# Optimization experiments

Measured on AMD Instinct MI355X. Metric: run time of the kernel, lower is better.

The kernel has to match this reference:

```python
import jax, jax.numpy as jnp
import numpy as np

N_NODES = 50000
N_EDGES = 800000
NODE_DIM = 64
EDGE_DIM = 32
OUT_FEATS = 64


def setup_inputs() -> dict:
    key = jax.random.key(0)
    k1, k2, k3, k4, k5, k6, k7 = jax.random.split(key, 7)
    node_features = jax.random.normal(k1, (N_NODES, NODE_DIM), dtype=jnp.float32)
    edge_features = jax.random.normal(k2, (N_EDGES, EDGE_DIM), dtype=jnp.float32)
    src = jax.random.randint(k3, (N_EDGES,), 0, N_NODES, dtype=jnp.int32)
    dst = jax.random.randint(k4, (N_EDGES,), 0, N_NODES, dtype=jnp.int32)
    in_dim = 2 * NODE_DIM + EDGE_DIM  # concat([e_ft, h_src, h_dst])
    w_group = jax.random.normal(k5, (in_dim,), dtype=jnp.float32) * 0.05
    w_srcattn = jax.random.normal(k6, (NODE_DIM + EDGE_DIM,), dtype=jnp.float32) * 0.05
    w_lin = jax.random.normal(k7, (in_dim, OUT_FEATS), dtype=jnp.float32) * 0.05
    return {"node_features": node_features, "edge_features": edge_features,
            "src": src, "dst": dst,
            "w_group": w_group, "w_srcattn": w_srcattn, "w_lin": w_lin}


def _segment_softmax(scores, seg, num_segments):
    # numerically-stable softmax of per-edge scalar scores within each segment
    m = jax.ops.segment_max(scores, seg, num_segments=num_segments)
    e = jnp.exp(scores - m[seg])
    s = jax.ops.segment_sum(e, seg, num_segments=num_segments)
    return e / s[seg]


def reference(node_features, edge_features, src, dst, w_group, w_srcattn, w_lin):
    h = node_features              # [N, node_dim]
    e_ft = edge_features           # [E, edge_dim]
    h_src = h[src]                 # [E, node_dim]
    h_dst = h[dst]                 # [E, node_dim]

    # --- group_apply_edges(group_by='src'): edge attention over out-edges of each src ---
    z2 = jnp.concatenate([e_ft, h_src, h_dst], axis=1)      # [E, edge_dim + 2*node_dim]
    a = z2 @ w_group                                        # [E]
    gamma = _segment_softmax(a, src, N_NODES)               # softmax over edges sharing src
    e_weighted = gamma[:, None] * e_ft                      # [E, edge_dim]

    # --- gnn_msg: msg = concat([h_src, e_weighted]) ---
    msg = jnp.concatenate([h_src, e_weighted], axis=1)      # [E, node_dim + edge_dim]

    # --- gnn_reduce: attention softmax over mailbox (edges sharing dst), weighted sum ---
    s = msg @ w_srcattn                                     # [E]
    alpha = _segment_softmax(s, dst, N_NODES)
    accum = jax.ops.segment_sum(alpha[:, None] * msg, dst, num_segments=N_NODES)  # [N, node_dim+edge_dim]

    # --- node_update: linear(concat([h, accum])) + relu ---
    h_cat = jnp.concatenate([h, accum], axis=1)             # [N, 2*node_dim + edge_dim]
    out = jax.nn.relu(h_cat @ w_lin)                        # [N, out_feats]
    return out
```

## Files before the change

### kernel.cpp

```cpp
#include <hip/hip_runtime.h>

#define NN 50000
#define NE 800000
#define NEB 3125
#define NHB 3125
#define NTILES 3125

typedef __attribute__((ext_vector_type(8))) short bf16x8;
typedef __attribute__((ext_vector_type(4))) short s16x4;
typedef __attribute__((ext_vector_type(4))) float f32x4;
typedef __attribute__((ext_vector_type(4))) int   i32x4;

static __device__ __forceinline__ short f2bf(float f) {
    unsigned int u = __float_as_uint(f);
    u += 0x7FFFu + ((u >> 16) & 1u);
    return (short)(u >> 16);
}
static __device__ __forceinline__ float bf2f(short b) {
    return __uint_as_float(((unsigned)(unsigned short)b) << 16);
}

__global__ __launch_bounds__(256) void k_pre(
    const float* __restrict__ h, const int* __restrict__ dst,
    const float* __restrict__ wg, const float* __restrict__ wa,
    int* __restrict__ cnt, int* __restrict__ rank,
    float* __restrict__ p1, float* __restrict__ pd, float* __restrict__ dpf,
    short* __restrict__ hb)
{
    int tid = threadIdx.x;
    if (blockIdx.x < NEB) {
        int e = blockIdx.x * 256 + tid;
        if (e < NE) rank[e] = atomicAdd(&cnt[dst[e]], 1);
        return;
    }
    __shared__ float4 ls[16], ld[16], lt[16];
    if (tid < 16)      ls[tid]      = ((const float4*)wg)[8 + tid];
    else if (tid < 32) ld[tid - 16] = ((const float4*)wg)[8 + tid];
    else if (tid < 48) lt[tid - 32] = ((const float4*)wa)[tid - 32];
    __syncthreads();
    int n = (blockIdx.x - NEB) * 16 + (tid >> 4);
    if (n >= NN) return;
    int l16 = tid & 15;
    float4 v = ((const float4*)(h + (size_t)n * 64))[l16];
    s16x4 hv;
    hv[0] = f2bf(v.x); hv[1] = f2bf(v.y); hv[2] = f2bf(v.z); hv[3] = f2bf(v.w);
    *(s16x4*)(hb + (size_t)n * 160 + l16 * 4) = hv;
    float4 w1 = ls[l16], w2 = ld[l16], w3 = lt[l16];
    float s1 = v.x*w1.x + v.y*w1.y + v.z*w1.z + v.w*w1.w;
    float s2 = v.x*w2.x + v.y*w2.y + v.z*w2.z + v.w*w2.w;
    float s3 = v.x*w3.x + v.y*w3.y + v.z*w3.z + v.w*w3.w;
    #pragma unroll
    for (int m = 8; m; m >>= 1) {
        s1 += __shfl_xor(s1, m);
        s2 += __shfl_xor(s2, m);
        s3 += __shfl_xor(s3, m);
    }
    if (l16 == 0) { p1[n] = s1; pd[n] = s2; dpf[2 * n + 1] = s3; }
}

__global__ __launch_bounds__(256) void k_assign(
    const int* __restrict__ cnt, int* __restrict__ off, int* __restrict__ gtotal,
    const float* __restrict__ wl, short* __restrict__ wlbT)
{
    if (blockIdx.x >= 196) {
        int idx = (blockIdx.x - 196) * 256 + threadIdx.x;
        int k = idx >> 6, nn = idx & 63;
        wlbT[nn * 160 + k] = f2bf(wl[idx]);
        return;
    }
    int n = blockIdx.x * 256 + threadIdx.x;
    int lane = threadIdx.x & 63;
    int c = (n < NN) ? cnt[n] : 0;
    int pre = c;
    #pragma unroll
    for (int d = 1; d < 64; d <<= 1) {
        int v = __shfl_up(pre, d);
        if (lane >= d) pre += v;
    }
    int base = 0;
    if (lane == 63) base = atomicAdd(gtotal, pre);
    base = __shfl(base, 63);
    if (n < NN) off[n] = base + pre - c;
}

__global__ __launch_bounds__(256) void k_edge(
    const float* __restrict__ ef, const int* __restrict__ src,
    const int* __restrict__ dst, const int* __restrict__ rank,
    const float* __restrict__ wg, const float* __restrict__ wa,
    const float* __restrict__ p1, const float* __restrict__ pd,
    float* __restrict__ dpf, const int* __restrict__ off,
    i32x4* __restrict__ recA)
{
    __shared__ float4 lwe[8], lae[8];
    int tid = threadIdx.x;
    if (tid < 8)       lwe[tid]     = ((const float4*)wg)[tid];
    else if (tid < 16) lae[tid - 8] = ((const float4*)wa)[tid - 8 + 16];
    __syncthreads();
    int e = blockIdx.x * 256 + tid;
    if (e >= NE) return;
    int s = src[e], d = dst[e], rk = rank[e];
    float p1v = p1[s], pdv = pd[d];
    int pos = off[d] + rk;
    const float4* e4 = (const float4*)(ef + (size_t)e * 32);
    float a = 0.f, u = 0.f;
    #pragma unroll
    for (int q = 0; q < 8; ++q) {
        float4 v = e4[q], w = lwe[q], w2 = lae[q];
        a += v.x*w.x  + v.y*w.y  + v.z*w.z  + v.w*w.w;
        u += v.x*w2.x + v.y*w2.y + v.z*w2.z + v.w*w2.w;
    }
    float ev = __expf(a + p1v + pdv);
    atomicAdd(&dpf[2 * s], ev);
    recA[pos] = (i32x4){s, e, __float_as_int(ev), __float_as_int(u)};
}

__global__ __launch_bounds__(256) void k_reduce(
    const float* __restrict__ ef, const int* __restrict__ cnt,
    const int* __restrict__ off, const float2* __restrict__ dp,
    const i32x4* __restrict__ recA, short* __restrict__ hb)
{
    int n = blockIdx.x * 4 + (threadIdx.x >> 6);
    if (n >= NN) return;
    int lane = threadIdx.x & 63;
    bool up = lane >= 32;
    int l5 = lane & 31;
    int deg = cnt[n], base = off[n];
    const i32x4* rp = recA + base;
    float acch = 0.f, acce = 0.f, den = 0.f;
    int j = 0;
    for (; j + 8 <= deg; j += 8) {
        i32x4 r[8];
        #pragma unroll
        for (int t = 0; t < 8; ++t) r[t] = rp[j + t];
        float2 dv[8]; float hv[8];
        #pragma unroll
        for (int t = 0; t < 8; ++t) {
            dv[t] = dp[r[t][0]];
            hv[t] = bf2f(hb[(size_t)(unsigned)r[t][0] * 160 + lane]);
        }
        float efv[4];
        #pragma unroll
        for (int t = 0; t < 4; ++t) {
            int ee = up ? r[2*t+1][1] : r[2*t][1];
            efv[t] = ef[((unsigned)ee << 5) + l5];
        }
        float g[8], s[8];
        #pragma unroll
        for (int t = 0; t < 8; ++t) {
            g[t] = __int_as_float(r[t][2]) * __builtin_amdgcn_rcpf(dv[t].x);
            s[t] = __expf(dv[t].y + g[t] * __int_as_float(r[t][3]));
            den  += s[t];
            acch += s[t] * hv[t];
        }
        #pragma unroll
        for (int t = 0; t < 4; ++t) {
            float w = up ? s[2*t+1]*g[2*t+1] : s[2*t]*g[2*t];
            acce += w * efv[t];
        }
    }
    if (j + 4 <= deg) {
        i32x4 r[4];
        #pragma unroll
        for (int t = 0; t < 4; ++t) r[t] = rp[j + t];
        float2 dv[4]; float hv[4];
        #pragma unroll
        for (int t = 0; t < 4; ++t) {
            dv[t] = dp[r[t][0]];
            hv[t] = bf2f(hb[(size_t)(unsigned)r[t][0] * 160 + lane]);
        }
        float efv[2];
        #pragma unroll
        for (int t = 0; t < 2; ++t) {
            int ee = up ? r[2*t+1][1] : r[2*t][1];
            efv[t] = ef[((unsigned)ee << 5) + l5];
        }
        float g[4], s[4];
        #pragma unroll
        for (int t = 0; t < 4; ++t) {
            g[t] = __int_as_float(r[t][2]) * __builtin_amdgcn_rcpf(dv[t].x);
            s[t] = __expf(dv[t].y + g[t] * __int_as_float(r[t][3]));
            den  += s[t];
            acch += s[t] * hv[t];
        }
        #pragma unroll
        for (int t = 0; t < 2; ++t) {
            float w = up ? s[2*t+1]*g[2*t+1] : s[2*t]*g[2*t];
            acce += w * efv[t];
        }
        j += 4;
    }
    for (; j < deg; ++j) {
        i32x4 r = rp[j];
        float2 dt = dp[r[0]];
        float g = __int_as_float(r[2]) * __builtin_amdgcn_rcpf(dt.x);
        float sx = __expf(dt.y + g * __int_as_float(r[3]));
        den += sx;
        acch += sx * bf2f(hb[(size_t)(unsigned)r[0] * 160 + lane]);
        if (!up) acce += sx * g * ef[((unsigned)r[1] << 5) + l5];
    }
    acce += __shfl_xor(acce, 32);
    float inv = (deg > 0) ? __builtin_amdgcn_rcpf(den) : 0.f;
    size_t hbase = (size_t)n * 160;
    hb[hbase + 64 + lane] = f2bf(acch * inv);
    if (!up) hb[hbase + 128 + l5] = f2bf(acce * inv);
}

__global__ __launch_bounds__(256) void k_node_update(
    const short* __restrict__ hb, const short* __restrict__ wlbT,
    float* __restrict__ out)
{
    int lane = threadIdx.x & 63;
    int col  = lane & 15;
    int quad = lane >> 4;
    int wid  = blockIdx.x * 4 + (threadIdx.x >> 6);
    int nwaves = gridDim.x * 4;

    bf16x8 bfr[5][4];
    #pragma unroll
    for (int nt = 0; nt < 4; ++nt) {
        const short* bp = wlbT + (size_t)(nt * 16 + col) * 160 + quad * 8;
        #pragma unroll
        for (int kc = 0; kc < 5; ++kc)
            bfr[kc][nt] = *(const bf16x8*)(bp + kc * 32);
    }

    for (int tile = wid; tile < NTILES; tile += nwaves) {
        int n = tile * 16 + col;
        f32x4 acc[4];
        #pragma unroll
        for (int nt = 0; nt < 4; ++nt) acc[nt] = (f32x4){0.f, 0.f, 0.f, 0.f};

        const short* hrow = hb + (size_t)n * 160 + quad * 8;
        #pragma unroll
        for (int kc = 0; kc < 5; ++kc) {
            bf16x8 af = *(const bf16x8*)(hrow + kc * 32);
            #pragma unroll
            for (int nt = 0; nt < 4; ++nt)
                acc[nt] = __builtin_amdgcn_mfma_f32_16x16x32_bf16(
                    af, bfr[kc][nt], acc[nt], 0, 0, 0);
        }

        #pragma unroll
        for (int nt = 0; nt < 4; ++nt) {
            #pragma unroll
            for (int r = 0; r < 4; ++r) {
                int node = tile * 16 + quad * 4 + r;
                out[(size_t)node * 64 + nt * 16 + col] = fmaxf(acc[nt][r], 0.f);
            }
        }
    }
}

extern "C" void kernel_launch(void* const* d_in, const int* in_sizes, int n_in,
                              void* d_out, int out_size, void* d_ws, size_t ws_size,
                              hipStream_t stream)
{
    const float* h   = (const float*)d_in[0];
    const float* ef  = (const float*)d_in[1];
    const int*   src = (const int*)d_in[2];
    const int*   dst = (const int*)d_in[3];
    const float* wg  = (const float*)d_in[4];
    const float* wa  = (const float*)d_in[5];
    const float* wl  = (const float*)d_in[6];
    float* out = (float*)d_out;

    float*  ws     = (float*)d_ws;
    float*  dpf    = ws;
    int*    cnt    = (int*)(ws + 2 * NN);
    int*    gtotal = (int*)(ws + 3 * NN);
    int*    off    = (int*)(ws + 3 * NN + 16);
    float*  p1     = ws + 4 * NN + 16;
    float*  pd     = ws + 5 * NN + 16;
    int*    rank   = (int*)(ws + 6 * NN + 16);
    short*  wlbT   = (short*)(ws + 6 * NN + 16 + NE);
    i32x4*  recA   = (i32x4*)(ws + 6 * NN + 16 + NE + 5120);
    short*  hb     = (short*)(ws + 6 * NN + 16 + 5 * NE + 5120);

    hipMemsetAsync(d_ws, 0, (size_t)(3 * NN + 16) * sizeof(float), stream);

    k_pre<<<NEB + NHB, 256, 0, stream>>>(h, dst, wg, wa, cnt, rank, p1, pd,
                                         dpf, hb);
    k_assign<<<236, 256, 0, stream>>>(cnt, off, gtotal, wl, wlbT);
    k_edge<<<NEB, 256, 0, stream>>>(ef, src, dst, rank, wg, wa, p1, pd, dpf,
                                    off, recA);
    k_reduce<<<(NN + 3) / 4, 256, 0, stream>>>(ef, cnt, off,
                                               (const float2*)dpf, recA, hb);
    k_node_update<<<391, 256, 0, stream>>>(hb, wlbT, out);
}
```

Measured before the change: 339.9 us.

## Split dst counting into eight byte-packed sub-counters to reduce atomic contention

Measured after the change: 418.1 us. +23.0%, slower.

```diff
diff --git a/kernel.cpp b/kernel.cpp
--- a/kernel.cpp
+++ b/kernel.cpp
@@ -5,6 +5,7 @@
 #define NEB 3125
 #define NHB 3125
 #define NTILES 3125
+#define NKEY (8 * NN)
 
 typedef __attribute__((ext_vector_type(8))) short bf16x8;
 typedef __attribute__((ext_vector_type(4))) short s16x4;
@@ -23,14 +24,18 @@
 __global__ __launch_bounds__(256) void k_pre(
     const float* __restrict__ h, const int* __restrict__ dst,
     const float* __restrict__ wg, const float* __restrict__ wa,
-    int* __restrict__ cnt, int* __restrict__ rank,
+    unsigned* __restrict__ cntP, int* __restrict__ rank,
     float* __restrict__ p1, float* __restrict__ pd, float* __restrict__ dpf,
     short* __restrict__ hb)
 {
     int tid = threadIdx.x;
     if (blockIdx.x < NEB) {
         int e = blockIdx.x * 256 + tid;
-        if (e < NE) rank[e] = atomicAdd(&cnt[dst[e]], 1);
+        int g = blockIdx.x & 7;
+        int key = g * NN + dst[e];
+        int sh = (key & 3) * 8;
+        unsigned old = atomicAdd(&cntP[key >> 2], 1u << sh);
+        rank[e] = (int)((old >> sh) & 255u);
         return;
     }
     __shared__ float4 ls[16], ld[16], lt[16];
@@ -59,18 +64,20 @@
 }
 
 __global__ __launch_bounds__(256) void k_assign(
-    const int* __restrict__ cnt, int* __restrict__ off, int* __restrict__ gtotal,
-    const float* __restrict__ wl, short* __restrict__ wlbT)
-{
-    if (blockIdx.x >= 196) {
-        int idx = (blockIdx.x - 196) * 256 + threadIdx.x;
+    const unsigned* __restrict__ cntP, int* __restrict__ offG,
+    int* __restrict__ gtotal, const float* __restrict__ wl,
+    short* __restrict__ wlbT)
+{
+    if (blockIdx.x >= 1563) {
+        int idx = (blockIdx.x - 1563) * 256 + threadIdx.x;
         int k = idx >> 6, nn = idx & 63;
         wlbT[nn * 160 + k] = f2bf(wl[idx]);
         return;
     }
-    int n = blockIdx.x * 256 + threadIdx.x;
+    int k = blockIdx.x * 256 + threadIdx.x;
     int lane = threadIdx.x & 63;
-    int c = (n < NN) ? cnt[n] : 0;
+    int c = 0;
+    if (k < NKEY) c = (int)((cntP[k >> 2] >> ((k & 3) * 8)) & 255u);
     int pre = c;
     #pragma unroll
     for (int d = 1; d < 64; d <<= 1) {
@@ -80,7 +87,7 @@
     int base = 0;
     if (lane == 63) base = atomicAdd(gtotal, pre);
     base = __shfl(base, 63);
-    if (n < NN) off[n] = base + pre - c;
+    if (k < NKEY) offG[k] = base + pre - c;
 }
 
 __global__ __launch_bounds__(256) void k_edge(
@@ -88,7 +95,7 @@
     const int* __restrict__ dst, const int* __restrict__ rank,
     const float* __restrict__ wg, const float* __restrict__ wa,
     const float* __restrict__ p1, const float* __restrict__ pd,
-    float* __restrict__ dpf, const int* __restrict__ off,
+    float* __restrict__ dpf, const int* __restrict__ offG,
     i32x4* __restrict__ recA)
 {
     __shared__ float4 lwe[8], lae[8];
@@ -97,10 +104,11 @@
     else if (tid < 16) lae[tid - 8] = ((const float4*)wa)[tid - 8 + 16];
     __syncthreads();
     int e = blockIdx.x * 256 + tid;
-    if (e >= NE) return;
+    int g = blockIdx.x & 7;
     int s = src[e], d = dst[e], rk = rank[e];
     float p1v = p1[s], pdv = pd[d];
-    int pos = off[d] + rk;
+    int pos = offG[g * NN + d] + rk;
+    pos = (pos < NE) ? pos : (NE - 1);
     const float4* e4 = (const float4*)(ef + (size_t)e * 32);
     float a = 0.f, u = 0.f;
     #pragma unroll
@@ -115,8 +123,8 @@
 }
 
 __global__ __launch_bounds__(256) void k_reduce(
-    const float* __restrict__ ef, const int* __restrict__ cnt,
-    const int* __restrict__ off, const float2* __restrict__ dp,
+    const float* __restrict__ ef, const unsigned* __restrict__ cntP,
+    const int* __restrict__ offG, const float2* __restrict__ dp,
     const i32x4* __restrict__ recA, short* __restrict__ hb)
 {
     int n = blockIdx.x * 4 + (threadIdx.x >> 6);
@@ -124,14 +132,31 @@
     int lane = threadIdx.x & 63;
     bool up = lane >= 32;
     int l5 = lane & 31;
-    int deg = cnt[n], base = off[n];
-    const i32x4* rp = recA + base;
+
+    int Pv[9]; int adj[8];
+    Pv[0] = 0;
+    #pragma unroll
+    for (int g = 0; g < 8; ++g) {
+        int key = g * NN + n;
+        int o = offG[key];
+        int c = (int)((cntP[key >> 2] >> ((key & 3) * 8)) & 255u);
+        Pv[g + 1] = Pv[g] + c;
+        adj[g] = o - Pv[g];
+    }
+    int deg = Pv[8];
+
     float acch = 0.f, acce = 0.f, den = 0.f;
     int j = 0;
     for (; j + 8 <= deg; j += 8) {
         i32x4 r[8];
         #pragma unroll
-        for (int t = 0; t < 8; ++t) r[t] = rp[j + t];
+        for (int t = 0; t < 8; ++t) {
+            int q = j + t;
+            int aq = adj[0];
+            #pragma unroll
+            for (int g = 1; g < 8; ++g) aq = (q >= Pv[g]) ? adj[g] : aq;
+            r[t] = recA[aq + q];
+        }
         float2 dv[8]; float hv[8];
         #pragma unroll
         for (int t = 0; t < 8; ++t) {
@@ -161,7 +186,13 @@
     if (j + 4 <= deg) {
         i32x4 r[4];
         #pragma unroll
-        for (int t = 0; t < 4; ++t) r[t] = rp[j + t];
+        for (int t = 0; t < 4; ++t) {
+            int q = j + t;
+            int aq = adj[0];
+            #pragma unroll
+            for (int g = 1; g < 8; ++g) aq = (q >= Pv[g]) ? adj[g] : aq;
+            r[t] = recA[aq + q];
+        }
         float2 dv[4]; float hv[4];
         #pragma unroll
         for (int t = 0; t < 4; ++t) {
@@ -190,13 +221,17 @@
         j += 4;
     }
     for (; j < deg; ++j) {
-        i32x4 r = rp[j];
+        int q = j;
+        int aq = adj[0];
+        #pragma unroll
+        for (int g = 1; g < 8; ++g) aq = (q >= Pv[g]) ? adj[g] : aq;
+        i32x4 r = recA[aq + q];
         float2 dt = dp[r[0]];
-        float g = __int_as_float(r[2]) * __builtin_amdgcn_rcpf(dt.x);
-        float sx = __expf(dt.y + g * __int_as_float(r[3]));
+        float gg = __int_as_float(r[2]) * __builtin_amdgcn_rcpf(dt.x);
+        float sx = __expf(dt.y + gg * __int_as_float(r[3]));
         den += sx;
         acch += sx * bf2f(hb[(size_t)(unsigned)r[0] * 160 + lane]);
-        if (!up) acce += sx * g * ef[((unsigned)r[1] << 5) + l5];
+        if (!up) acce += sx * gg * ef[((unsigned)r[1] << 5) + l5];
     }
     acce += __shfl_xor(acce, 32);
     float inv = (deg > 0) ? __builtin_amdgcn_rcpf(den) : 0.f;
@@ -264,26 +299,26 @@
     const float* wl  = (const float*)d_in[6];
     float* out = (float*)d_out;
 
-    float*  ws     = (float*)d_ws;
-    float*  dpf    = ws;
-    int*    cnt    = (int*)(ws + 2 * NN);
-    int*    gtotal = (int*)(ws + 3 * NN);
-    int*    off    = (int*)(ws + 3 * NN + 16);
-    float*  p1     = ws + 4 * NN + 16;
-    float*  pd     = ws + 5 * NN + 16;
-    int*    rank   = (int*)(ws + 6 * NN + 16);
-    short*  wlbT   = (short*)(ws + 6 * NN + 16 + NE);
-    i32x4*  recA   = (i32x4*)(ws + 6 * NN + 16 + NE + 5120);
-    short*  hb     = (short*)(ws + 6 * NN + 16 + 5 * NE + 5120);
-
-    hipMemsetAsync(d_ws, 0, (size_t)(3 * NN + 16) * sizeof(float), stream);
-
-    k_pre<<<NEB + NHB, 256, 0, stream>>>(h, dst, wg, wa, cnt, rank, p1, pd,
+    float*    ws     = (float*)d_ws;
+    float*    dpf    = ws;
+    unsigned* cntP   = (unsigned*)(ws + 2 * NN);
+    int*      gtotal = (int*)(ws + 4 * NN);
+    int*      offG   = (int*)(ws + 4 * NN + 16);
+    float*    p1     = ws + 12 * NN + 16;
+    float*    pd     = ws + 13 * NN + 16;
+    int*      rank   = (int*)(ws + 14 * NN + 16);
+    short*    wlbT   = (short*)(ws + 14 * NN + 16 + NE);
+    i32x4*    recA   = (i32x4*)(ws + 14 * NN + 16 + NE + 5120);
+    short*    hb     = (short*)(ws + 14 * NN + 16 + 5 * NE + 5120);
+
+    hipMemsetAsync(d_ws, 0, (size_t)(4 * NN + 16) * sizeof(float), stream);
+
+    k_pre<<<NEB + NHB, 256, 0, stream>>>(h, dst, wg, wa, cntP, rank, p1, pd,
                                          dpf, hb);
-    k_assign<<<236, 256, 0, stream>>>(cnt, off, gtotal, wl, wlbT);
+    k_assign<<<1603, 256, 0, stream>>>(cntP, offG, gtotal, wl, wlbT);
     k_edge<<<NEB, 256, 0, stream>>>(ef, src, dst, rank, wg, wa, p1, pd, dpf,
-                                    off, recA);
-    k_reduce<<<(NN + 3) / 4, 256, 0, stream>>>(ef, cnt, off,
+                                    offG, recA);
+    k_reduce<<<(NN + 3) / 4, 256, 0, stream>>>(ef, cntP, offG,
                                                (const float2*)dpf, recA, hb);
     k_node_update<<<391, 256, 0, stream>>>(hb, wlbT, out);
 }
```
